# Optimization experiments

Measured on AMD Instinct MI355X. Metric: run time of the kernel, lower is better.

## Reference

```python
import jax, jax.numpy as jnp
import numpy as np

MI, DIS, DIN, HID, L, H, NG, H1, OUT = 2048, 1024, 3072, 256, 15, 8, 8, 512, 64
DENOM = 4.0 / 7.0  # (grid_max - grid_min) / (num_grids - 1)
EPS = 1e-5


def _ln(x, g, b):
    m = jnp.mean(x, axis=-1, keepdims=True)
    v = jnp.mean((x - m) ** 2, axis=-1, keepdims=True)
    return (x - m) * jax.lax.rsqrt(v + EPS) * g + b


def _fastkan(x, ln_g, ln_b, grid, Ws, Wb, bb):
    xn = _ln(x, ln_g, ln_b)
    basis = jnp.exp(-(((xn[..., None] - grid) / DENOM) ** 2))  # [N, DIN, NG]
    ret = basis.reshape(x.shape[0], -1) @ Ws.T                  # SplineLinear (no bias)
    return ret + jax.nn.silu(x) @ Wb.T + bb                      # base update


def _hgcn(x, G, W, attn, bias, rW1, rb1, rW2, rb2, ln_g, ln_b, jk_W, jk_b):
    # per-layer multi-head conv: mean_h a_h * G @ (x @ W_h) == G @ (x @ (sum_h a_h W_h / H))
    def step(xc, p):
        W_l, a_l, b_l, rW1_l, rb1_l, rW2_l, rb2_l, g_l, be_l = p
        W_eff = jnp.einsum('h,hio->io', a_l, W_l) / H
        out = G @ (xc @ W_eff) + b_l
        gate = jax.nn.sigmoid(jax.nn.relu(out @ rW1_l.T + rb1_l) @ rW2_l.T + rb2_l)
        out = _ln(out * gate, g_l, be_l)
        out = jnp.where(out >= 0, out, 0.25 * out)  # leaky_relu(0.25); dropout off (eval)
        return out, out
    _, outs = jax.lax.scan(step, x, (W, attn, bias, rW1, rb1, rW2, rb2, ln_g, ln_b))
    jk = jnp.moveaxis(outs, 0, 1).reshape(x.shape[0], L * HID)   # jumping-knowledge concat
    return jk @ jk_W.T + jk_b


def _mlp3(x, W1, b1, W2, b2, W3, b3):
    h = jax.nn.relu(x @ W1.T + b1)
    h = jax.nn.relu(h @ W2.T + b2)
    return jax.nn.relu(h @ W3.T + b3)


def _forward(concat_mi, concat_dis, G_mi, G_dis, AT, A, rbf_grid, mi_kan_ln_g, mi_kan_ln_b, mi_kan_Ws, mi_kan_Wb, mi_kan_bb, dis_kan_ln_g, dis_kan_ln_b, dis_kan_Ws, dis_kan_Wb, dis_kan_bb, mi_W, mi_attn, mi_bias, mi_rW1, mi_rb1, mi_rW2, mi_rb2, mi_ln_g, mi_ln_b, mi_jk_W, mi_jk_b, dis_W, dis_attn, dis_bias, dis_rW1, dis_rb1, dis_rW2, dis_rb2, dis_ln_g, dis_ln_b, dis_jk_W, dis_jk_b, lx_W1, lx_b1, lx_W2, lx_b2, lx_W3, lx_b3, ly_W1, ly_b1, ly_W2, ly_b2, ly_W3, ly_b3, ne_W, ne_b, he_W, he_b, mun_W, mun_b, mue_W, mue_b):
    # AT and A are accepted by the original forward but never used in its body.
    mi_e = _fastkan(concat_mi, mi_kan_ln_g, mi_kan_ln_b, rbf_grid, mi_kan_Ws, mi_kan_Wb, mi_kan_bb)
    dis_e = _fastkan(concat_dis, dis_kan_ln_g, dis_kan_ln_b, rbf_grid, dis_kan_Ws, dis_kan_Wb, dis_kan_bb)
    mi_f = _hgcn(mi_e, G_mi, mi_W, mi_attn, mi_bias, mi_rW1, mi_rb1, mi_rW2, mi_rb2, mi_ln_g, mi_ln_b, mi_jk_W, mi_jk_b)
    dis_f = _hgcn(dis_e, G_dis, dis_W, dis_attn, dis_bias, dis_rW1, dis_rb1, dis_rW2, dis_rb2, dis_ln_g, dis_ln_b, dis_jk_W, dis_jk_b)
    x = _mlp3(mi_f, lx_W1, lx_b1, lx_W2, lx_b2, lx_W3, lx_b3)
    y = _mlp3(dis_f, ly_W1, ly_b1, ly_W2, ly_b2, ly_W3, ly_b3)
    result_h = x @ y.T                                           # [MI, DIS]
    z_node = jax.nn.relu(concat_mi @ ne_W.T + ne_b)              # node_encoders1 (eval: no dropout)
    z_edge = jax.nn.relu(concat_dis @ he_W.T + he_b)             # hyperedge_encoders1
    z_node_mean = z_node @ mun_W.T + mun_b                       # _enc_mu_node (identity act)
    z_edge_mean = z_edge @ mue_W.T + mue_b                       # _enc_mu_hedge
    recon = z_node_mean @ z_edge_mean.T                          # decoder2 with identity act
    score = 0.7 * jax.nn.sigmoid(recon) + 0.3 * jax.nn.sigmoid(result_h)
    return score, recon


def setup_inputs() -> dict:
    ks = iter(jax.random.split(jax.random.key(0), 96))
    nrm = lambda shape, s: jax.random.normal(next(ks), shape, dtype=jnp.float32) * s
    uni = lambda shape: jax.random.uniform(next(ks), shape, dtype=jnp.float32)
    d = {}
    d['concat_mi'] = nrm((MI, DIN), 1.0)
    d['concat_dis'] = nrm((DIS, DIN), 1.0)
    d['G_mi'] = uni((MI, MI)) / MI    # row-normalized dense hypergraph adjacency
    d['G_dis'] = uni((DIS, DIS)) / DIS
    d['AT'] = uni((DIS, MI))
    d['A'] = uni((MI, DIS))
    d['rbf_grid'] = jnp.linspace(-2.0, 2.0, NG).astype(jnp.float32)
    for p in ('mi', 'dis'):
        d[p + '_kan_ln_g'] = jnp.ones((DIN,), jnp.float32)
        d[p + '_kan_ln_b'] = jnp.zeros((DIN,), jnp.float32)
        d[p + '_kan_Ws'] = nrm((HID, DIN * NG), 0.02)
        d[p + '_kan_Wb'] = nrm((HID, DIN), 0.02)
        d[p + '_kan_bb'] = nrm((HID,), 0.01)
        d[p + '_W'] = nrm((L, H, HID, HID), 0.06)
        d[p + '_attn'] = jnp.ones((L, H), jnp.float32)
        d[p + '_bias'] = nrm((L, HID), 0.01)
        d[p + '_rW1'] = nrm((L, HID // 4, HID), 0.05)
        d[p + '_rb1'] = nrm((L, HID // 4), 0.01)
        d[p + '_rW2'] = nrm((L, HID, HID // 4), 0.05)
        d[p + '_rb2'] = nrm((L, HID), 0.01)
        d[p + '_ln_g'] = jnp.ones((L, HID), jnp.float32)
        d[p + '_ln_b'] = jnp.zeros((L, HID), jnp.float32)
        d[p + '_jk_W'] = nrm((HID, L * HID), 0.02)
        d[p + '_jk_b'] = nrm((HID,), 0.01)
    for p in ('lx', 'ly'):
        d[p + '_W1'] = nrm((256, HID), 0.05); d[p + '_b1'] = nrm((256,), 0.01)
        d[p + '_W2'] = nrm((128, 256), 0.05); d[p + '_b2'] = nrm((128,), 0.01)
        d[p + '_W3'] = nrm((64, 128), 0.05); d[p + '_b3'] = nrm((64,), 0.01)
    d['ne_W'] = nrm((H1, DIN), 0.02); d['ne_b'] = nrm((H1,), 0.01)
    d['he_W'] = nrm((H1, DIN), 0.02); d['he_b'] = nrm((H1,), 0.01)
    d['mun_W'] = nrm((OUT, H1), 0.02); d['mun_b'] = nrm((OUT,), 0.01)
    d['mue_W'] = nrm((OUT, H1), 0.02); d['mue_b'] = nrm((OUT,), 0.01)
    return d


def reference(concat_mi, concat_dis, G_mi, G_dis, AT, A, rbf_grid, mi_kan_ln_g, mi_kan_ln_b, mi_kan_Ws, mi_kan_Wb, mi_kan_bb, dis_kan_ln_g, dis_kan_ln_b, dis_kan_Ws, dis_kan_Wb, dis_kan_bb, mi_W, mi_attn, mi_bias, mi_rW1, mi_rb1, mi_rW2, mi_rb2, mi_ln_g, mi_ln_b, mi_jk_W, mi_jk_b, dis_W, dis_attn, dis_bias, dis_rW1, dis_rb1, dis_rW2, dis_rb2, dis_ln_g, dis_ln_b, dis_jk_W, dis_jk_b, lx_W1, lx_b1, lx_W2, lx_b2, lx_W3, lx_b3, ly_W1, ly_b1, ly_W2, ly_b2, ly_W3, ly_b3, ne_W, ne_b, he_W, he_b, mun_W, mun_b, mue_W, mue_b):
    return _forward(concat_mi, concat_dis, G_mi, G_dis, AT, A, rbf_grid, mi_kan_ln_g, mi_kan_ln_b, mi_kan_Ws, mi_kan_Wb, mi_kan_bb, dis_kan_ln_g, dis_kan_ln_b, dis_kan_Ws, dis_kan_Wb, dis_kan_bb, mi_W, mi_attn, mi_bias, mi_rW1, mi_rb1, mi_rW2, mi_rb2, mi_ln_g, mi_ln_b, mi_jk_W, mi_jk_b, dis_W, dis_attn, dis_bias, dis_rW1, dis_rb1, dis_rW2, dis_rb2, dis_ln_g, dis_ln_b, dis_jk_W, dis_jk_b, lx_W1, lx_b1, lx_W2, lx_b2, lx_W3, lx_b3, ly_W1, ly_b1, ly_W2, ly_b2, ly_W3, ly_b3, ne_W, ne_b, he_W, he_b, mun_W, mun_b, mue_W, mue_b)
```

## Files before the change

kernel.cpp:

```cpp
#include <hip/hip_runtime.h>
#include <cstdint>
#include <cstddef>

typedef unsigned short u16;
typedef __attribute__((ext_vector_type(8))) short short8;
typedef __attribute__((ext_vector_type(4))) float f32x4;

#define MI_N  2048
#define DIS_N 1024
#define TOT_N 3072
#define DIN   3072
#define HID   256
#define LL    15
#define NG    8

__device__ __forceinline__ float b2f(u16 u) {
  unsigned int v = ((unsigned int)u) << 16;
  float f;
  __builtin_memcpy(&f, &v, 4);
  return f;
}
__device__ __forceinline__ u16 f2b(float f) {
  unsigned int u;
  __builtin_memcpy(&u, &f, 4);
  u = (u + 0x7fffu + ((u >> 16) & 1u)) >> 16;
  return (u16)u;
}
__device__ __forceinline__ float sigf(float x) { return 1.f / (1.f + __expf(-x)); }

#define NSEG 20
struct CvtJobs {
  const float* src[NSEG];
  u16* dst[NSEG];
  int nblk[NSEG];
  int nseg;
};

__global__ __launch_bounds__(256) void cvt_f2b(CvtJobs j) {
  int b = blockIdx.x, s = 0;
  while (s + 1 < j.nseg && b >= j.nblk[s]) { b -= j.nblk[s]; ++s; }
  const long base = ((long)b * 256 + threadIdx.x) * 8;
  const float4 v0 = *(const float4*)(j.src[s] + base);
  const float4 v1 = *(const float4*)(j.src[s] + base + 4);
  short8 o;
  o[0] = (short)f2b(v0.x); o[1] = (short)f2b(v0.y);
  o[2] = (short)f2b(v0.z); o[3] = (short)f2b(v0.w);
  o[4] = (short)f2b(v1.x); o[5] = (short)f2b(v1.y);
  o[6] = (short)f2b(v1.z); o[7] = (short)f2b(v1.w);
  *(short8*)(j.dst[s] + base) = o;
}

struct GP {
  const u16* A; int lda;
  const u16* B; int ldb;
  void* C; int ldc;
  const float* bias;
  int K;
  int mblk;
};

template <int ACT, int TRANS, int F32OUT, int NCT>
__global__ __launch_bounds__(256) void gemm_bt(GP p0, GP p1) {
  GP p = p0;
  int bx = blockIdx.x;
  if (bx >= p0.mblk) { bx -= p0.mblk; p = p1; }
  const int tid = threadIdx.x;
  const int w = tid >> 6;
  const int lane = tid & 63;
  const int m16 = lane & 15, quad = lane >> 4;
  const int kph = quad * 8;
  const long row0 = (long)bx * 32 + m16;
  const long colBase = (long)blockIdx.y * (16 * NCT);
  f32x4 acc[2][NCT] = {};
  const u16* A0 = p.A + row0 * (long)p.lda + kph;
  const u16* A1 = A0 + 16L * p.lda;
  const u16* Bb = p.B + (colBase + m16) * (long)p.ldb + kph;
  const long bstep = 16L * p.ldb;
  for (int kk = w * 32; kk < p.K; kk += 128) {
    short8 a0 = *(const short8*)(A0 + kk);
    short8 a1 = *(const short8*)(A1 + kk);
#pragma unroll
    for (int c = 0; c < NCT; ++c) {
      short8 b = *(const short8*)(Bb + c * bstep + kk);
      acc[0][c] = __builtin_amdgcn_mfma_f32_16x16x32_bf16(a0, b, acc[0][c], 0, 0, 0);
      acc[1][c] = __builtin_amdgcn_mfma_f32_16x16x32_bf16(a1, b, acc[1][c], 0, 0, 0);
    }
  }
  __shared__ float red[2][64][NCT * 8 + 1];
  float* av = (float*)acc;
  if (w >= 2) {
#pragma unroll
    for (int i = 0; i < NCT * 8; ++i) red[w - 2][lane][i] = av[i];
  }
  __syncthreads();
  if (w < 2) {
#pragma unroll
    for (int i = 0; i < NCT * 8; ++i) av[i] += red[w][lane][i];
  }
  __syncthreads();
  if (w == 1) {
#pragma unroll
    for (int i = 0; i < NCT * 8; ++i) red[0][lane][i] = av[i];
  }
  __syncthreads();
  if (w != 0) return;
#pragma unroll
  for (int i = 0; i < NCT * 8; ++i) av[i] += red[0][lane][i];
#pragma unroll
  for (int c = 0; c < NCT; ++c) {
    const long col = colBase + c * 16 + m16;
    const float bv = p.bias ? p.bias[col] : 0.f;
#pragma unroll
    for (int r = 0; r < 2; ++r) {
      const long orow = (long)bx * 32 + r * 16 + quad * 4;
#pragma unroll
      for (int j = 0; j < 4; ++j) {
        float v = acc[r][c][j] + bv;
        if (ACT == 1) v = fmaxf(v, 0.f);
        if (ACT == 2) v = sigf(v);
        if (F32OUT)
          ((float*)p.C)[(orow + j) * (long)p.ldc + col] = v;
        else if (TRANS)
          ((u16*)p.C)[col * (long)p.ldc + orow + j] = f2b(v);
        else
          ((u16*)p.C)[(orow + j) * (long)p.ldc + col] = f2b(v);
      }
    }
  }
}

struct FKP {
  const u16* xn; const u16* xb;
  const u16* Ws; const u16* Wb;
  float* partial;
  int rowoff;
  int mblk;
};

__global__ __launch_bounds__(256) void fastkan_gemm(FKP p0, FKP p1, const float* grid8) {
  FKP p = p0;
  int bx = blockIdx.x;
  if (bx >= p0.mblk) { bx -= p0.mblk; p = p1; }
  const int chunk = blockIdx.z;
  const int tid = threadIdx.x;
  const int w = tid >> 6;
  const int lane = tid & 63;
  const int m16 = lane & 15, quad = lane >> 4, kph = quad * 8;
  const long row0 = (long)bx * 32 + m16;
  const long colBase = (long)blockIdx.y * 128;
  f32x4 acc[2][8] = {};
  if (chunk < 4) {
    float gv[8];
#pragma unroll
    for (int j = 0; j < 8; ++j) gv[j] = grid8[j];
    const u16* xn0 = p.xn + row0 * (long)DIN;
    const u16* xn1 = xn0 + 16L * DIN;
    const int k0 = chunk * 6144, k1 = k0 + 6144;
    for (int kk = k0 + w * 32; kk < k1; kk += 128) {
      const int d = (kk >> 3) + quad;
      const float x0 = b2f(xn0[d]);
      const float x1 = b2f(xn1[d]);
      short8 a0, a1;
#pragma unroll
      for (int j = 0; j < 8; ++j) {
        float t0 = (x0 - gv[j]) * 1.75f;
        float t1 = (x1 - gv[j]) * 1.75f;
        a0[j] = (short)f2b(__expf(-t0 * t0));
        a1[j] = (short)f2b(__expf(-t1 * t1));
      }
#pragma unroll
      for (int c = 0; c < 8; ++c) {
        const u16* Bp = p.Ws + (colBase + c * 16 + m16) * (long)(DIN * NG) + kk + kph;
        short8 b = *(const short8*)Bp;
        acc[0][c] = __builtin_amdgcn_mfma_f32_16x16x32_bf16(a0, b, acc[0][c], 0, 0, 0);
        acc[1][c] = __builtin_amdgcn_mfma_f32_16x16x32_bf16(a1, b, acc[1][c], 0, 0, 0);
      }
    }
  } else {
    const u16* x0p = p.xb + row0 * (long)DIN + kph;
    const u16* x1p = x0p + 16L * DIN;
    for (int kk = w * 32; kk < DIN; kk += 128) {
      short8 r0 = *(const short8*)(x0p + kk);
      short8 r1 = *(const short8*)(x1p + kk);
      short8 a0, a1;
#pragma unroll
      for (int j = 0; j < 8; ++j) {
        float v0 = b2f((u16)r0[j]);
        float v1 = b2f((u16)r1[j]);
        a0[j] = (short)f2b(v0 * sigf(v0));
        a1[j] = (short)f2b(v1 * sigf(v1));
      }
#pragma unroll
      for (int c = 0; c < 8; ++c) {
        const u16* Bp = p.Wb + (colBase + c * 16 + m16) * (long)DIN + kk + kph;
        short8 b = *(const short8*)Bp;
        acc[0][c] = __builtin_amdgcn_mfma_f32_16x16x32_bf16(a0, b, acc[0][c], 0, 0, 0);
        acc[1][c] = __builtin_amdgcn_mfma_f32_16x16x32_bf16(a1, b, acc[1][c], 0, 0, 0);
      }
    }
  }
  __shared__ float red[2][64][65];
  float* av = (float*)acc;
  if (w >= 2) {
#pragma unroll
    for (int i = 0; i < 64; ++i) red[w - 2][lane][i] = av[i];
  }
  __syncthreads();
  if (w < 2) {
#pragma unroll
    for (int i = 0; i < 64; ++i) av[i] += red[w][lane][i];
  }
  __syncthreads();
  if (w == 1) {
#pragma unroll
    for (int i = 0; i < 64; ++i) red[0][lane][i] = av[i];
  }
  __syncthreads();
  if (w != 0) return;
#pragma unroll
  for (int i = 0; i < 64; ++i) av[i] += red[0][lane][i];
  float* outp = p.partial + ((long)chunk * TOT_N + p.rowoff) * HID;
#pragma unroll
  for (int c = 0; c < 8; ++c) {
    const long col = colBase + c * 16 + m16;
#pragma unroll
    for (int r = 0; r < 2; ++r) {
      const long orow = (long)bx * 32 + r * 16 + quad * 4;
#pragma unroll
      for (int j = 0; j < 4; ++j) outp[(orow + j) * HID + col] = acc[r][c][j];
    }
  }
}

__global__ __launch_bounds__(256) void fk_combine(const float* partial, const float* bb_mi,
                                                  const float* bb_dis, u16* e) {
  const long i = (long)blockIdx.x * 256 + threadIdx.x;
  const int c = (int)(i & 255);
  const long n = i >> 8;
  float s = 0.f;
#pragma unroll
  for (int pI = 0; pI < 5; ++pI) s += partial[(long)pI * TOT_N * HID + i];
  s += (n < MI_N ? bb_mi : bb_dis)[c];
  e[i] = f2b(s);
}

struct HLP {
  const u16* G; const u16* t1t; u16* t1t_next; const u16* weff_next;
  const float* bias; const u16* rw1; const float* rb1;
  const u16* rw2; const float* rb2; const float* lng; const float* lnb;
  u16* jk; int M; int mblk;
};

__global__ __launch_bounds__(256) void hgcn_layer(HLP p0, HLP p1) {
  HLP p = p0;
  int bx = blockIdx.x;
  if (bx >= p0.mblk) { bx -= p0.mblk; p = p1; }
  const int tid = threadIdx.x;
  const int w = tid >> 6, lane = tid & 63;
  const int m16 = lane & 15, quad = lane >> 4, kph = quad * 8;
  const int cb = w * 64;
  const long row0 = (long)bx * 32;
  __shared__ __align__(16) u16 hl[32][264];
  __shared__ __align__(16) u16 gl[32][264];
  __shared__ __align__(16) u16 g1l[32][72];

  {
    f32x4 acc[2][4] = {};
    const u16* A0 = p.G + (row0 + m16) * (long)p.M + kph;
    const u16* A1 = A0 + 16L * p.M;
    const u16* Bb = p.t1t + (long)(cb + m16) * p.M + kph;
    const long bstep = 16L * p.M;
    for (int kk = 0; kk < p.M; kk += 32) {
      short8 a0 = *(const short8*)(A0 + kk);
      short8 a1 = *(const short8*)(A1 + kk);
#pragma unroll
      for (int c = 0; c < 4; ++c) {
        short8 b = *(const short8*)(Bb + c * bstep + kk);
        acc[0][c] = __builtin_amdgcn_mfma_f32_16x16x32_bf16(a0, b, acc[0][c], 0, 0, 0);
        acc[1][c] = __builtin_amdgcn_mfma_f32_16x16x32_bf16(a1, b, acc[1][c], 0, 0, 0);
      }
    }
#pragma unroll
    for (int c = 0; c < 4; ++c) {
      const int col = cb + c * 16 + m16;
      const float bv = p.bias[col];
#pragma unroll
      for (int r = 0; r < 2; ++r) {
        const int orow = r * 16 + quad * 4;
#pragma unroll
        for (int j = 0; j < 4; ++j) hl[orow + j][col] = f2b(acc[r][c][j] + bv);
      }
    }
  }
  __syncthreads();
  {
    f32x4 acc[2] = {};
    const u16* Bb = p.rw1 + (long)(w * 16 + m16) * 256 + kph;
#pragma unroll
    for (int kk = 0; kk < 256; kk += 32) {
      short8 a0 = *(const short8*)&hl[m16][kk + kph];
      short8 a1 = *(const short8*)&hl[16 + m16][kk + kph];
      short8 b = *(const short8*)(Bb + kk);
      acc[0] = __builtin_amdgcn_mfma_f32_16x16x32_bf16(a0, b, acc[0], 0, 0, 0);
      acc[1] = __builtin_amdgcn_mfma_f32_16x16x32_bf16(a1, b, acc[1], 0, 0, 0);
    }
    const int col = w * 16 + m16;
    const float bv = p.rb1[col];
#pragma unroll
    for (int r = 0; r < 2; ++r) {
      const int orow = r * 16 + quad * 4;
#pragma unroll
      for (int j = 0; j < 4; ++j) g1l[orow + j][col] = f2b(fmaxf(acc[r][j] + bv, 0.f));
    }
  }
  __syncthreads();
  {
    f32x4 acc[2][4] = {};
    const u16* Bb = p.rw2 + (long)(cb + m16) * 64 + kph;
#pragma unroll
    for (int kk = 0; kk < 64; kk += 32) {
      short8 a0 = *(const short8*)&g1l[m16][kk + kph];
      short8 a1 = *(const short8*)&g1l[16 + m16][kk + kph];
#pragma unroll
      for (int c = 0; c < 4; ++c) {
        short8 b = *(const short8*)(Bb + c * (16L * 64) + kk);
        acc[0][c] = __builtin_amdgcn_mfma_f32_16x16x32_bf16(a0, b, acc[0][c], 0, 0, 0);
        acc[1][c] = __builtin_amdgcn_mfma_f32_16x16x32_bf16(a1, b, acc[1][c], 0, 0, 0);
      }
    }
#pragma unroll
    for (int c = 0; c < 4; ++c) {
      const int col = cb + c * 16 + m16;
      const float bv = p.rb2[col];
#pragma unroll
      for (int r = 0; r < 2; ++r) {
        const int orow = r * 16 + quad * 4;
#pragma unroll
        for (int j = 0; j < 4; ++j) gl[orow + j][col] = f2b(sigf(acc[r][c][j] + bv));
      }
    }
  }
  __syncthreads();
  {
    const int row = tid >> 3;
    const int sub = tid & 7;
    float pv[32];
    float s1 = 0.f, s2 = 0.f;
#pragma unroll
    for (int i = 0; i < 32; ++i) {
      const int col = sub * 32 + i;
      const float v = b2f(hl[row][col]) * b2f(gl[row][col]);
      pv[i] = v; s1 += v; s2 += v * v;
    }
#pragma unroll
    for (int o = 1; o < 8; o <<= 1) { s1 += __shfl_xor(s1, o); s2 += __shfl_xor(s2, o); }
    const float m = s1 * (1.f / HID);
    const float inv = rsqrtf(s2 * (1.f / HID) - m * m + 1e-5f);
    u16* jrow = p.jk + (row0 + row) * (long)(LL * HID);
#pragma unroll
    for (int i = 0; i < 32; ++i) {
      const int col = sub * 32 + i;
      float y = (pv[i] - m) * inv * p.lng[col] + p.lnb[col];
      y = (y >= 0.f) ? y : 0.25f * y;
      const u16 yb = f2b(y);
      jrow[col] = yb;
      gl[row][col] = yb;
    }
  }
  if (!p.weff_next) return;
  __syncthreads();
  {
    f32x4 acc[2][4] = {};
    const u16* Bb = p.weff_next + (long)(cb + m16) * 256 + kph;
#pragma unroll
    for (int kk = 0; kk < 256; kk += 32) {
      short8 a0 = *(const short8*)&gl[m16][kk + kph];
      short8 a1 = *(const short8*)&gl[16 + m16][kk + kph];
#pragma unroll
      for (int c = 0; c < 4; ++c) {
        short8 b = *(const short8*)(Bb + c * (16L * 256) + kk);
        acc[0][c] = __builtin_amdgcn_mfma_f32_16x16x32_bf16(a0, b, acc[0][c], 0, 0, 0);
        acc[1][c] = __builtin_amdgcn_mfma_f32_16x16x32_bf16(a1, b, acc[1][c], 0, 0, 0);
      }
    }
#pragma unroll
    for (int c = 0; c < 4; ++c) {
      const long col = cb + c * 16 + m16;
#pragma unroll
      for (int r = 0; r < 2; ++r) {
        const int orow = r * 16 + quad * 4;
#pragma unroll
        for (int j = 0; j < 4; ++j)
          p.t1t_next[col * (long)p.M + row0 + orow + j] = f2b(acc[r][c][j]);
      }
    }
  }
}

__global__ __launch_bounds__(256) void weff_kernel(const float* Wmi, const float* Ami,
                                                   const float* Wdis, const float* Adis,
                                                   u16* outT) {
  const int b = blockIdx.x;
  const int s = b / 3840;
  const int r = b % 3840;
  const int l = r >> 8;
  const int t = r & 255;
  const int i0 = (t >> 4) << 4;
  const int o0 = (t & 15) << 4;
  const float* W = (s ? Wdis : Wmi) + (long)l * 8 * 65536;
  const float* A = (s ? Adis : Ami) + l * 8;
  const int tx = threadIdx.x & 15;
  const int ty = threadIdx.x >> 4;
  float sum = 0.f;
#pragma unroll
  for (int h = 0; h < 8; ++h)
    sum += A[h] * W[(long)h * 65536 + (long)(i0 + ty) * 256 + o0 + tx];
  sum *= 0.125f;
  __shared__ float tile[16][17];
  tile[ty][tx] = sum;
  __syncthreads();
  outT[((long)s * LL + l) * 65536 + (long)(o0 + ty) * 256 + i0 + tx] = f2b(tile[tx][ty]);
}

__device__ __forceinline__ void breduce2(float& a, float& b) {
  for (int o = 32; o > 0; o >>= 1) {
    a += __shfl_down(a, o);
    b += __shfl_down(b, o);
  }
  __shared__ float sm[8];
  const int w = threadIdx.x >> 6;
  const int lane = threadIdx.x & 63;
  if (lane == 0) { sm[w] = a; sm[4 + w] = b; }
  __syncthreads();
  if (threadIdx.x == 0) {
    sm[0] = sm[0] + sm[1] + sm[2] + sm[3];
    sm[4] = sm[4] + sm[5] + sm[6] + sm[7];
  }
  __syncthreads();
  a = sm[0];
  b = sm[4];
}

__global__ __launch_bounds__(256) void ln_silu(const float* xmi, const float* xdis,
                                               const float* gmi, const float* bmi,
                                               const float* gdis, const float* bdis,
                                               u16* xn, u16* cbf) {
  const int n = blockIdx.x;
  const bool ds = (n >= MI_N);
  const float* x = ds ? xdis + (long)(n - MI_N) * DIN : xmi + (long)n * DIN;
  const float* g = ds ? gdis : gmi;
  const float* be = ds ? bdis : bmi;
  float xv[12];
  float s1 = 0.f, s2 = 0.f;
#pragma unroll
  for (int j = 0; j < 12; ++j) {
    xv[j] = x[j * 256 + threadIdx.x];
    s1 += xv[j];
    s2 += xv[j] * xv[j];
  }
  breduce2(s1, s2);
  const float m = s1 * (1.f / DIN);
  const float inv = rsqrtf(s2 * (1.f / DIN) - m * m + 1e-5f);
#pragma unroll
  for (int j = 0; j < 12; ++j) {
    const int e = j * 256 + threadIdx.x;
    xn[(long)n * DIN + e] = f2b((xv[j] - m) * inv * g[e] + be[e]);
    cbf[(long)n * DIN + e] = f2b(xv[j]);
  }
}

__global__ __launch_bounds__(256) void final_combine(const float* rh, float* out) {
  const long i = (long)blockIdx.x * 256 + threadIdx.x;
  const float rc = out[(long)MI_N * DIS_N + i];
  out[i] = 0.7f * sigf(rc) + 0.3f * sigf(rh[i]);
}

extern "C" void kernel_launch(void* const* d_in, const int* in_sizes, int n_in,
                              void* d_out, int out_size, void* d_ws, size_t ws_size,
                              hipStream_t stream) {
  const float* concat_mi   = (const float*)d_in[0];
  const float* concat_dis  = (const float*)d_in[1];
  const float* G_mi        = (const float*)d_in[2];
  const float* G_dis       = (const float*)d_in[3];
  const float* rbf_grid    = (const float*)d_in[6];
  const float* mi_kan_ln_g = (const float*)d_in[7];
  const float* mi_kan_ln_b = (const float*)d_in[8];
  const float* mi_kan_Ws   = (const float*)d_in[9];
  const float* mi_kan_Wb   = (const float*)d_in[10];
  const float* mi_kan_bb   = (const float*)d_in[11];
  const float* mi_W        = (const float*)d_in[12];
  const float* mi_attn     = (const float*)d_in[13];
  const float* mi_bias     = (const float*)d_in[14];
  const float* mi_rW1      = (const float*)d_in[15];
  const float* mi_rb1      = (const float*)d_in[16];
  const float* mi_rW2      = (const float*)d_in[17];
  const float* mi_rb2      = (const float*)d_in[18];
  const float* mi_ln_g     = (const float*)d_in[19];
  const float* mi_ln_b     = (const float*)d_in[20];
  const float* mi_jk_W     = (const float*)d_in[21];
  const float* mi_jk_b     = (const float*)d_in[22];
  const float* dis_kan_ln_g = (const float*)d_in[23];
  const float* dis_kan_ln_b = (const float*)d_in[24];
  const float* dis_kan_Ws  = (const float*)d_in[25];
  const float* dis_kan_Wb  = (const float*)d_in[26];
  const float* dis_kan_bb  = (const float*)d_in[27];
  const float* dis_W       = (const float*)d_in[28];
  const float* dis_attn    = (const float*)d_in[29];
  const float* dis_bias    = (const float*)d_in[30];
  const float* dis_rW1     = (const float*)d_in[31];
  const float* dis_rb1     = (const float*)d_in[32];
  const float* dis_rW2     = (const float*)d_in[33];
  const float* dis_rb2     = (const float*)d_in[34];
  const float* dis_ln_g    = (const float*)d_in[35];
  const float* dis_ln_b    = (const float*)d_in[36];
  const float* dis_jk_W    = (const float*)d_in[37];
  const float* dis_jk_b    = (const float*)d_in[38];
  const float* lx_W1 = (const float*)d_in[39]; const float* lx_b1 = (const float*)d_in[40];
  const float* lx_W2 = (const float*)d_in[41]; const float* lx_b2 = (const float*)d_in[42];
  const float* lx_W3 = (const float*)d_in[43]; const float* lx_b3 = (const float*)d_in[44];
  const float* ly_W1 = (const float*)d_in[45]; const float* ly_b1 = (const float*)d_in[46];
  const float* ly_W2 = (const float*)d_in[47]; const float* ly_b2 = (const float*)d_in[48];
  const float* ly_W3 = (const float*)d_in[49]; const float* ly_b3 = (const float*)d_in[50];
  const float* ne_W  = (const float*)d_in[51]; const float* ne_b  = (const float*)d_in[52];
  const float* he_W  = (const float*)d_in[53]; const float* he_b  = (const float*)d_in[54];
  const float* mun_W = (const float*)d_in[55]; const float* mun_b = (const float*)d_in[56];
  const float* mue_W = (const float*)d_in[57]; const float* mue_b = (const float*)d_in[58];

  char* wp = (char*)d_ws;
  size_t off = 0;
  auto alloc = [&](size_t bytes) -> void* {
    void* p = wp + off;
    off += (bytes + 255) & ~(size_t)255;
    return p;
  };
  u16* cbf    = (u16*)alloc((size_t)TOT_N * DIN * 2);
  u16* gmib   = (u16*)alloc((size_t)MI_N * MI_N * 2);
  u16* gdisb  = (u16*)alloc((size_t)DIS_N * DIS_N * 2);
  u16* wsb0   = (u16*)alloc((size_t)256 * 24576 * 2);
  u16* wsb1   = (u16*)alloc((size_t)256 * 24576 * 2);
  u16* wbb0   = (u16*)alloc((size_t)256 * 3072 * 2);
  u16* wbb1   = (u16*)alloc((size_t)256 * 3072 * 2);
  u16* jkwb0  = (u16*)alloc((size_t)256 * 3840 * 2);
  u16* jkwb1  = (u16*)alloc((size_t)256 * 3840 * 2);
  u16* rw1b0  = (u16*)alloc((size_t)LL * 64 * 256 * 2);
  u16* rw1b1  = (u16*)alloc((size_t)LL * 64 * 256 * 2);
  u16* rw2b0  = (u16*)alloc((size_t)LL * 256 * 64 * 2);
  u16* rw2b1  = (u16*)alloc((size_t)LL * 256 * 64 * 2);
  u16* lxw1b  = (u16*)alloc((size_t)256 * 256 * 2);
  u16* lxw2b  = (u16*)alloc((size_t)128 * 256 * 2);
  u16* lxw3b  = (u16*)alloc((size_t)64 * 128 * 2);
  u16* lyw1b  = (u16*)alloc((size_t)256 * 256 * 2);
  u16* lyw2b  = (u16*)alloc((size_t)128 * 256 * 2);
  u16* lyw3b  = (u16*)alloc((size_t)64 * 128 * 2);
  u16* neb    = (u16*)alloc((size_t)512 * 3072 * 2);
  u16* heb    = (u16*)alloc((size_t)512 * 3072 * 2);
  u16* munb   = (u16*)alloc((size_t)64 * 512 * 2);
  u16* mueb   = (u16*)alloc((size_t)64 * 512 * 2);
  u16* wefft  = (u16*)alloc((size_t)2 * LL * 65536 * 2);
  u16* e      = (u16*)alloc((size_t)TOT_N * HID * 2);
  u16* t1t    = (u16*)alloc((size_t)HID * TOT_N * 2);
  u16* t1t2   = (u16*)alloc((size_t)HID * TOT_N * 2);
  u16* jk     = (u16*)alloc((size_t)TOT_N * LL * HID * 2);
  u16* fb     = (u16*)alloc((size_t)TOT_N * HID * 2);
  char* regA  = (char*)alloc(35000000);
  u16* xn     = (u16*)regA;
  float* fkp  = (float*)(regA + 18874624);
  u16* h1b    = (u16*)regA;
  u16* h2b    = (u16*)(regA + 1572864);
  u16* xyb    = (u16*)(regA + 2359296);
  float* rh   = (float*)(regA + 2752512);
  u16* zb     = (u16*)(regA + 11141120);
  u16* zm     = (u16*)(regA + 14286848);
  float* outf = (float*)d_out;
  float* rec  = outf + (size_t)MI_N * DIS_N;
  (void)ws_size; (void)in_sizes; (void)n_in; (void)out_size;

  const dim3 B256(256);

  {
    CvtJobs cj{};
    int ns = 0, total = 0;
    auto push = [&](const float* s, u16* dst, int count) {
      cj.src[ns] = s; cj.dst[ns] = dst; cj.nblk[ns] = count / 2048;
      total += count / 2048; ++ns;
    };
    push(G_mi, gmib, MI_N * MI_N);
    push(G_dis, gdisb, DIS_N * DIS_N);
    push(mi_kan_Ws, wsb0, 256 * 24576);
    push(dis_kan_Ws, wsb1, 256 * 24576);
    push(mi_kan_Wb, wbb0, 256 * 3072);
    push(dis_kan_Wb, wbb1, 256 * 3072);
    push(mi_jk_W, jkwb0, 256 * 3840);
    push(dis_jk_W, jkwb1, 256 * 3840);
    push(mi_rW1, rw1b0, LL * 64 * 256);
    push(dis_rW1, rw1b1, LL * 64 * 256);
    push(mi_rW2, rw2b0, LL * 256 * 64);
    push(dis_rW2, rw2b1, LL * 256 * 64);
    push(lx_W1, lxw1b, 256 * 256);
    push(lx_W2, lxw2b, 128 * 256);
    push(lx_W3, lxw3b, 64 * 128);
    push(ly_W1, lyw1b, 256 * 256);
    push(ly_W2, lyw2b, 128 * 256);
    push(ly_W3, lyw3b, 64 * 128);
    push(ne_W, neb, 512 * 3072);
    push(he_W, heb, 512 * 3072);
    cj.nseg = ns;
    cvt_f2b<<<dim3(total), B256, 0, stream>>>(cj);
    CvtJobs cj2{};
    cj2.src[0] = mun_W; cj2.dst[0] = munb; cj2.nblk[0] = (64 * 512) / 2048;
    cj2.src[1] = mue_W; cj2.dst[1] = mueb; cj2.nblk[1] = (64 * 512) / 2048;
    cj2.nseg = 2;
    cvt_f2b<<<dim3(32), B256, 0, stream>>>(cj2);
  }
  ln_silu<<<dim3(TOT_N), B256, 0, stream>>>(concat_mi, concat_dis, mi_kan_ln_g, mi_kan_ln_b,
                                            dis_kan_ln_g, dis_kan_ln_b, xn, cbf);
  weff_kernel<<<dim3(2 * LL * 256), B256, 0, stream>>>(mi_W, mi_attn, dis_W, dis_attn, wefft);
  {
    FKP f0{xn, cbf, wsb0, wbb0, fkp, 0, 64};
    FKP f1{xn + (size_t)MI_N * DIN, cbf + (size_t)MI_N * DIN, wsb1, wbb1, fkp, MI_N, 32};
    fastkan_gemm<<<dim3(96, 2, 5), B256, 0, stream>>>(f0, f1, rbf_grid);
    fk_combine<<<dim3(TOT_N * HID / 256), B256, 0, stream>>>(fkp, mi_kan_bb, dis_kan_bb, e);
  }
  {
    GP a0{e, HID, wefft, 256, t1t, MI_N, nullptr, 256, 64};
    GP a1{e + (size_t)MI_N * HID, HID, wefft + (size_t)LL * 65536, 256,
          t1t + (size_t)HID * MI_N, DIS_N, nullptr, 256, 32};
    gemm_bt<0, 1, 0, 4><<<dim3(96, 4), B256, 0, stream>>>(a0, a1);
  }
  {
    u16* tc = t1t;
    u16* tn = t1t2;
    for (int l = 0; l < LL; ++l) {
      const bool last = (l == LL - 1);
      HLP h0{gmib, tc, tn, last ? nullptr : wefft + (size_t)(l + 1) * 65536,
             mi_bias + l * HID, rw1b0 + (size_t)l * 64 * HID, mi_rb1 + l * 64,
             rw2b0 + (size_t)l * HID * 64, mi_rb2 + l * HID,
             mi_ln_g + l * HID, mi_ln_b + l * HID, jk + (size_t)l * HID, MI_N, 64};
      HLP h1{gdisb, tc + (size_t)HID * MI_N, tn + (size_t)HID * MI_N,
             last ? nullptr : wefft + ((size_t)LL + l + 1) * 65536,
             dis_bias + l * HID, rw1b1 + (size_t)l * 64 * HID, dis_rb1 + l * 64,
             rw2b1 + (size_t)l * HID * 64, dis_rb2 + l * HID,
             dis_ln_g + l * HID, dis_ln_b + l * HID,
             jk + (size_t)MI_N * LL * HID + (size_t)l * HID, DIS_N, 32};
      hgcn_layer<<<dim3(96), B256, 0, stream>>>(h0, h1);
      u16* t = tc; tc = tn; tn = t;
    }
  }
  {
    GP j0{jk, LL * HID, jkwb0, LL * HID, fb, HID, mi_jk_b, LL * HID, 64};
    GP j1{jk + (size_t)MI_N * LL * HID, LL * HID, jkwb1, LL * HID, fb + (size_t)MI_N * HID,
          HID, dis_jk_b, LL * HID, 32};
    gemm_bt<0, 0, 0, 4><<<dim3(96, 4), B256, 0, stream>>>(j0, j1);
  }
  {
    GP m0{fb, HID, lxw1b, HID, h1b, 256, lx_b1, HID, 64};
    GP m1{fb + (size_t)MI_N * HID, HID, lyw1b, HID, h1b + (size_t)MI_N * 256, 256, ly_b1,
          HID, 32};
    gemm_bt<1, 0, 0, 4><<<dim3(96, 4), B256, 0, stream>>>(m0, m1);
    GP n0{h1b, 256, lxw2b, 256, h2b, 128, lx_b2, 256, 64};
    GP n1{h1b + (size_t)MI_N * 256, 256, lyw2b, 256, h2b + (size_t)MI_N * 128, 128, ly_b2,
          256, 32};
    gemm_bt<1, 0, 0, 4><<<dim3(96, 2), B256, 0, stream>>>(n0, n1);
    GP o0{h2b, 128, lxw3b, 128, xyb, 64, lx_b3, 128, 64};
    GP o1{h2b + (size_t)MI_N * 128, 128, lyw3b, 128, xyb + (size_t)MI_N * 64, 64, ly_b3,
          128, 32};
    gemm_bt<1, 0, 0, 4><<<dim3(96, 1), B256, 0, stream>>>(o0, o1);
  }
  {
    GP r0{xyb, 64, xyb + (size_t)MI_N * 64, 64, rh, DIS_N, nullptr, 64, 64};
    gemm_bt<0, 0, 1, 4><<<dim3(64, 16), B256, 0, stream>>>(r0, r0);
  }
  {
    GP e0{cbf, DIN, neb, DIN, zb, 512, ne_b, DIN, 64};
    GP e1{cbf + (size_t)MI_N * DIN, DIN, heb, DIN, zb + (size_t)MI_N * 512, 512, he_b, DIN,
          32};
    gemm_bt<1, 0, 0, 4><<<dim3(96, 8), B256, 0, stream>>>(e0, e1);
  }
  {
    GP u0{zb, 512, munb, 512, zm, 64, mun_b, 512, 64};
    GP u1{zb + (size_t)MI_N * 512, 512, mueb, 512, zm + (size_t)MI_N * 64, 64, mue_b, 512,
          32};
    gemm_bt<0, 0, 0, 4><<<dim3(96, 1), B256, 0, stream>>>(u0, u1);
  }
  {
    GP c0{zm, 64, zm + (size_t)MI_N * 64, 64, rec, DIS_N, nullptr, 64, 64};
    gemm_bt<0, 0, 1, 4><<<dim3(64, 16), B256, 0, stream>>>(c0, c0);
  }
  final_combine<<<dim3(MI_N * DIS_N / 256), B256, 0, stream>>>(rh, outf);
}
```

Before: 1.613 ms.

## Fuse all HGCN layers into one persistent cooperative kernel with grid barriers

Replaces the 15 per-layer hgcn_layer launches with a single cooperative kernel that loops over layers and uses an atomic grid barrier between them. Work is split into 192 blocks of 16 rows instead of 96 blocks of 32 rows, and the big G@t1 GEMM is split along K across the four waves, followed by an LDS reduction. The aim is to remove launch overhead and raise parallelism. In exchange it adds barrier cost, extra LDS reduction traffic and a spin-wait, and it relies on all blocks being co-resident if the plain-launch fallback is used.

```diff
diff --git a/kernel.cpp b/kernel.cpp
--- a/kernel.cpp
+++ b/kernel.cpp
@@ -13,6 +13,7 @@
 #define HID   256
 #define LL    15
 #define NG    8
+#define NBLK  192
 
 __device__ __forceinline__ float b2f(u16 u) {
   unsigned int v = ((unsigned int)u) << 16;
@@ -244,156 +245,202 @@
   e[i] = f2b(s);
 }
 
-struct HLP {
-  const u16* G; const u16* t1t; u16* t1t_next; const u16* weff_next;
-  const float* bias; const u16* rw1; const float* rb1;
-  const u16* rw2; const float* rb2; const float* lng; const float* lnb;
-  u16* jk; int M; int mblk;
+struct CoopP {
+  const u16* gmi; const u16* gdis; const u16* wefft;
+  u16* t1a; u16* t1b;
+  const float* bias_mi; const float* bias_dis;
+  const u16* rw1_mi; const u16* rw1_dis;
+  const u16* rw2_mi; const u16* rw2_dis;
+  const float* rb1_mi; const float* rb1_dis;
+  const float* rb2_mi; const float* rb2_dis;
+  const float* lng_mi; const float* lng_dis;
+  const float* lnb_mi; const float* lnb_dis;
+  u16* jk;
+  unsigned* bar;
 };
 
-__global__ __launch_bounds__(256) void hgcn_layer(HLP p0, HLP p1) {
-  HLP p = p0;
-  int bx = blockIdx.x;
-  if (bx >= p0.mblk) { bx -= p0.mblk; p = p1; }
+__device__ __forceinline__ void grid_sync(unsigned* bar) {
+  __syncthreads();
+  if (threadIdx.x == 0) {
+    __threadfence();
+    const unsigned g = atomicAdd(&bar[1], 0u);
+    const unsigned a = atomicAdd(&bar[0], 1u) + 1u;
+    if (a == (unsigned)NBLK) {
+      atomicExch(&bar[0], 0u);
+      atomicAdd(&bar[1], 1u);
+    } else {
+      while (atomicAdd(&bar[1], 0u) == g) __builtin_amdgcn_s_sleep(8);
+    }
+    __threadfence();
+  }
+  __syncthreads();
+}
+
+__global__ __launch_bounds__(256) void hgcn_all(CoopP p) {
+  const int b = blockIdx.x;
   const int tid = threadIdx.x;
   const int w = tid >> 6, lane = tid & 63;
   const int m16 = lane & 15, quad = lane >> 4, kph = quad * 8;
   const int cb = w * 64;
-  const long row0 = (long)bx * 32;
-  __shared__ __align__(16) u16 hl[32][264];
-  __shared__ __align__(16) u16 gl[32][264];
-  __shared__ __align__(16) u16 g1l[32][72];
-
-  {
-    f32x4 acc[2][4] = {};
-    const u16* A0 = p.G + (row0 + m16) * (long)p.M + kph;
-    const u16* A1 = A0 + 16L * p.M;
-    const u16* Bb = p.t1t + (long)(cb + m16) * p.M + kph;
-    const long bstep = 16L * p.M;
-    for (int kk = 0; kk < p.M; kk += 32) {
-      short8 a0 = *(const short8*)(A0 + kk);
-      short8 a1 = *(const short8*)(A1 + kk);
+  const bool mi = (b < 128);
+  const int M = mi ? MI_N : DIS_N;
+  const int row0 = mi ? b * 16 : (b - 128) * 16;
+  const long grow = mi ? row0 : (long)MI_N + row0;
+  const u16* G = mi ? p.gmi : p.gdis;
+
+  __shared__ float red[2][64][65];
+  __shared__ __align__(16) u16 hl[16][264];
+  __shared__ __align__(16) u16 g1l[16][72];
+  __shared__ __align__(16) u16 gl[16][264];
+
+  u16* tc = p.t1a;
+  u16* tn = p.t1b;
+
+  for (int l = 0; l < LL; ++l) {
+    const float* bias = (mi ? p.bias_mi : p.bias_dis) + l * HID;
+    const u16* rw1 = (mi ? p.rw1_mi : p.rw1_dis) + (size_t)l * 64 * HID;
+    const float* rb1 = (mi ? p.rb1_mi : p.rb1_dis) + l * 64;
+    const u16* rw2 = (mi ? p.rw2_mi : p.rw2_dis) + (size_t)l * HID * 64;
+    const float* rb2 = (mi ? p.rb2_mi : p.rb2_dis) + l * HID;
+    const float* lng = (mi ? p.lng_mi : p.lng_dis) + l * HID;
+    const float* lnb = (mi ? p.lnb_mi : p.lnb_dis) + l * HID;
+    const u16* tb = mi ? tc : tc + (size_t)HID * MI_N;
+
+    {
+      f32x4 acc[16] = {};
+      const u16* A = G + (long)(row0 + m16) * M + kph;
+      const u16* Bc = tb + (long)m16 * M + kph;
+      const int kbase = w * (M >> 2);
+      const int it1 = M >> 7;
+#pragma unroll 4
+      for (int kk = 0; kk < it1; ++kk) {
+        const int ka = kbase + kk * 32;
+        short8 a = *(const short8*)(A + ka);
+#pragma unroll
+        for (int c = 0; c < 16; ++c) {
+          short8 bb = *(const short8*)(Bc + (long)c * 16 * M + ka);
+          acc[c] = __builtin_amdgcn_mfma_f32_16x16x32_bf16(a, bb, acc[c], 0, 0, 0);
+        }
+      }
+      float* av = (float*)acc;
+      if (w >= 2) {
+#pragma unroll
+        for (int i = 0; i < 64; ++i) red[w - 2][lane][i] = av[i];
+      }
+      __syncthreads();
+      if (w < 2) {
+#pragma unroll
+        for (int i = 0; i < 64; ++i) av[i] += red[w][lane][i];
+      }
+      __syncthreads();
+      if (w == 1) {
+#pragma unroll
+        for (int i = 0; i < 64; ++i) red[0][lane][i] = av[i];
+      }
+      __syncthreads();
+      if (w == 0) {
+#pragma unroll
+        for (int i = 0; i < 64; ++i) av[i] += red[0][lane][i];
+#pragma unroll
+        for (int c = 0; c < 16; ++c) {
+          const int col = c * 16 + m16;
+          const float bv = bias[col];
+#pragma unroll
+          for (int j = 0; j < 4; ++j) hl[quad * 4 + j][col] = f2b(acc[c][j] + bv);
+        }
+      }
+      __syncthreads();
+    }
+    {
+      f32x4 acc = {};
+      const u16* Bb = rw1 + (long)(w * 16 + m16) * 256 + kph;
+#pragma unroll
+      for (int kk = 0; kk < 256; kk += 32) {
+        short8 a = *(const short8*)&hl[m16][kk + kph];
+        short8 bb = *(const short8*)(Bb + kk);
+        acc = __builtin_amdgcn_mfma_f32_16x16x32_bf16(a, bb, acc, 0, 0, 0);
+      }
+      const int col = w * 16 + m16;
+      const float bv = rb1[col];
+#pragma unroll
+      for (int j = 0; j < 4; ++j) g1l[quad * 4 + j][col] = f2b(fmaxf(acc[j] + bv, 0.f));
+    }
+    __syncthreads();
+    {
+      f32x4 acc[4] = {};
+      const u16* Bb = rw2 + (long)(cb + m16) * 64 + kph;
+#pragma unroll
+      for (int kk = 0; kk < 64; kk += 32) {
+        short8 a = *(const short8*)&g1l[m16][kk + kph];
+#pragma unroll
+        for (int c = 0; c < 4; ++c) {
+          short8 bb = *(const short8*)(Bb + c * (16L * 64) + kk);
+          acc[c] = __builtin_amdgcn_mfma_f32_16x16x32_bf16(a, bb, acc[c], 0, 0, 0);
+        }
+      }
 #pragma unroll
       for (int c = 0; c < 4; ++c) {
-        short8 b = *(const short8*)(Bb + c * bstep + kk);
-        acc[0][c] = __builtin_amdgcn_mfma_f32_16x16x32_bf16(a0, b, acc[0][c], 0, 0, 0);
-        acc[1][c] = __builtin_amdgcn_mfma_f32_16x16x32_bf16(a1, b, acc[1][c], 0, 0, 0);
-      }
-    }
-#pragma unroll
-    for (int c = 0; c < 4; ++c) {
-      const int col = cb + c * 16 + m16;
-      const float bv = p.bias[col];
-#pragma unroll
-      for (int r = 0; r < 2; ++r) {
-        const int orow = r * 16 + quad * 4;
-#pragma unroll
-        for (int j = 0; j < 4; ++j) hl[orow + j][col] = f2b(acc[r][c][j] + bv);
-      }
-    }
-  }
-  __syncthreads();
-  {
-    f32x4 acc[2] = {};
-    const u16* Bb = p.rw1 + (long)(w * 16 + m16) * 256 + kph;
-#pragma unroll
-    for (int kk = 0; kk < 256; kk += 32) {
-      short8 a0 = *(const short8*)&hl[m16][kk + kph];
-      short8 a1 = *(const short8*)&hl[16 + m16][kk + kph];
-      short8 b = *(const short8*)(Bb + kk);
-      acc[0] = __builtin_amdgcn_mfma_f32_16x16x32_bf16(a0, b, acc[0], 0, 0, 0);
-      acc[1] = __builtin_amdgcn_mfma_f32_16x16x32_bf16(a1, b, acc[1], 0, 0, 0);
-    }
-    const int col = w * 16 + m16;
-    const float bv = p.rb1[col];
-#pragma unroll
-    for (int r = 0; r < 2; ++r) {
-      const int orow = r * 16 + quad * 4;
-#pragma unroll
-      for (int j = 0; j < 4; ++j) g1l[orow + j][col] = f2b(fmaxf(acc[r][j] + bv, 0.f));
-    }
-  }
-  __syncthreads();
-  {
-    f32x4 acc[2][4] = {};
-    const u16* Bb = p.rw2 + (long)(cb + m16) * 64 + kph;
-#pragma unroll
-    for (int kk = 0; kk < 64; kk += 32) {
-      short8 a0 = *(const short8*)&g1l[m16][kk + kph];
-      short8 a1 = *(const short8*)&g1l[16 + m16][kk + kph];
+        const int col = cb + c * 16 + m16;
+        const float bv = rb2[col];
+#pragma unroll
+        for (int j = 0; j < 4; ++j) gl[quad * 4 + j][col] = f2b(sigf(acc[c][j] + bv));
+      }
+    }
+    __syncthreads();
+    {
+      const int row = tid >> 4, sub = tid & 15;
+      float pv[16];
+      float s1 = 0.f, s2 = 0.f;
+#pragma unroll
+      for (int i = 0; i < 16; ++i) {
+        const int col = sub * 16 + i;
+        const float v = b2f(hl[row][col]) * b2f(gl[row][col]);
+        pv[i] = v; s1 += v; s2 += v * v;
+      }
+#pragma unroll
+      for (int o = 1; o < 16; o <<= 1) {
+        s1 += __shfl_xor(s1, o);
+        s2 += __shfl_xor(s2, o);
+      }
+      const float m = s1 * (1.f / HID);
+      const float inv = rsqrtf(s2 * (1.f / HID) - m * m + 1e-5f);
+      u16* jrow = p.jk + (size_t)(grow + row) * (LL * HID) + (size_t)l * HID;
+#pragma unroll
+      for (int i = 0; i < 16; ++i) {
+        const int col = sub * 16 + i;
+        float y = (pv[i] - m) * inv * lng[col] + lnb[col];
+        y = (y >= 0.f) ? y : 0.25f * y;
+        const u16 yb = f2b(y);
+        jrow[col] = yb;
+        gl[row][col] = yb;
+      }
+    }
+    if (l == LL - 1) break;
+    __syncthreads();
+    {
+      const u16* weff_nx = p.wefft + ((mi ? 0 : LL) + l + 1) * (size_t)65536;
+      u16* to = mi ? tn : tn + (size_t)HID * MI_N;
+      f32x4 acc[4] = {};
+      const u16* Bb = weff_nx + (long)(cb + m16) * 256 + kph;
+#pragma unroll
+      for (int kk = 0; kk < 256; kk += 32) {
+        short8 a = *(const short8*)&gl[m16][kk + kph];
+#pragma unroll
+        for (int c = 0; c < 4; ++c) {
+          short8 bb = *(const short8*)(Bb + c * (16L * 256) + kk);
+          acc[c] = __builtin_amdgcn_mfma_f32_16x16x32_bf16(a, bb, acc[c], 0, 0, 0);
+        }
+      }
 #pragma unroll
       for (int c = 0; c < 4; ++c) {
-        short8 b = *(const short8*)(Bb + c * (16L * 64) + kk);
-        acc[0][c] = __builtin_amdgcn_mfma_f32_16x16x32_bf16(a0, b, acc[0][c], 0, 0, 0);
-        acc[1][c] = __builtin_amdgcn_mfma_f32_16x16x32_bf16(a1, b, acc[1][c], 0, 0, 0);
-      }
-    }
-#pragma unroll
-    for (int c = 0; c < 4; ++c) {
-      const int col = cb + c * 16 + m16;
-      const float bv = p.rb2[col];
-#pragma unroll
-      for (int r = 0; r < 2; ++r) {
-        const int orow = r * 16 + quad * 4;
-#pragma unroll
-        for (int j = 0; j < 4; ++j) gl[orow + j][col] = f2b(sigf(acc[r][c][j] + bv));
-      }
-    }
-  }
-  __syncthreads();
-  {
-    const int row = tid >> 3;
-    const int sub = tid & 7;
-    float pv[32];
-    float s1 = 0.f, s2 = 0.f;
-#pragma unroll
-    for (int i = 0; i < 32; ++i) {
-      const int col = sub * 32 + i;
-      const float v = b2f(hl[row][col]) * b2f(gl[row][col]);
-      pv[i] = v; s1 += v; s2 += v * v;
-    }
-#pragma unroll
-    for (int o = 1; o < 8; o <<= 1) { s1 += __shfl_xor(s1, o); s2 += __shfl_xor(s2, o); }
-    const float m = s1 * (1.f / HID);
-    const float inv = rsqrtf(s2 * (1.f / HID) - m * m + 1e-5f);
-    u16* jrow = p.jk + (row0 + row) * (long)(LL * HID);
-#pragma unroll
-    for (int i = 0; i < 32; ++i) {
-      const int col = sub * 32 + i;
-      float y = (pv[i] - m) * inv * p.lng[col] + p.lnb[col];
-      y = (y >= 0.f) ? y : 0.25f * y;
-      const u16 yb = f2b(y);
-      jrow[col] = yb;
-      gl[row][col] = yb;
-    }
-  }
-  if (!p.weff_next) return;
-  __syncthreads();
-  {
-    f32x4 acc[2][4] = {};
-    const u16* Bb = p.weff_next + (long)(cb + m16) * 256 + kph;
-#pragma unroll
-    for (int kk = 0; kk < 256; kk += 32) {
-      short8 a0 = *(const short8*)&gl[m16][kk + kph];
-      short8 a1 = *(const short8*)&gl[16 + m16][kk + kph];
-#pragma unroll
-      for (int c = 0; c < 4; ++c) {
-        short8 b = *(const short8*)(Bb + c * (16L * 256) + kk);
-        acc[0][c] = __builtin_amdgcn_mfma_f32_16x16x32_bf16(a0, b, acc[0][c], 0, 0, 0);
-        acc[1][c] = __builtin_amdgcn_mfma_f32_16x16x32_bf16(a1, b, acc[1][c], 0, 0, 0);
-      }
-    }
-#pragma unroll
-    for (int c = 0; c < 4; ++c) {
-      const long col = cb + c * 16 + m16;
-#pragma unroll
-      for (int r = 0; r < 2; ++r) {
-        const int orow = r * 16 + quad * 4;
+        const long col = cb + c * 16 + m16;
 #pragma unroll
         for (int j = 0; j < 4; ++j)
-          p.t1t_next[col * (long)p.M + row0 + orow + j] = f2b(acc[r][c][j]);
-      }
-    }
+          to[col * (long)M + row0 + quad * 4 + j] = f2b(acc[c][j]);
+      }
+    }
+    grid_sync(p.bar);
+    u16* t = tc; tc = tn; tn = t;
   }
 }
 
@@ -562,6 +609,7 @@
   u16* t1t2   = (u16*)alloc((size_t)HID * TOT_N * 2);
   u16* jk     = (u16*)alloc((size_t)TOT_N * LL * HID * 2);
   u16* fb     = (u16*)alloc((size_t)TOT_N * HID * 2);
+  unsigned* barp = (unsigned*)alloc(256);
   char* regA  = (char*)alloc(35000000);
   u16* xn     = (u16*)regA;
   float* fkp  = (float*)(regA + 18874624);
@@ -628,22 +676,16 @@
     gemm_bt<0, 1, 0, 4><<<dim3(96, 4), B256, 0, stream>>>(a0, a1);
   }
   {
-    u16* tc = t1t;
-    u16* tn = t1t2;
-    for (int l = 0; l < LL; ++l) {
-      const bool last = (l == LL - 1);
-      HLP h0{gmib, tc, tn, last ? nullptr : wefft + (size_t)(l + 1) * 65536,
-             mi_bias + l * HID, rw1b0 + (size_t)l * 64 * HID, mi_rb1 + l * 64,
-             rw2b0 + (size_t)l * HID * 64, mi_rb2 + l * HID,
-             mi_ln_g + l * HID, mi_ln_b + l * HID, jk + (size_t)l * HID, MI_N, 64};
-      HLP h1{gdisb, tc + (size_t)HID * MI_N, tn + (size_t)HID * MI_N,
-             last ? nullptr : wefft + ((size_t)LL + l + 1) * 65536,
-             dis_bias + l * HID, rw1b1 + (size_t)l * 64 * HID, dis_rb1 + l * 64,
-             rw2b1 + (size_t)l * HID * 64, dis_rb2 + l * HID,
-             dis_ln_g + l * HID, dis_ln_b + l * HID,
-             jk + (size_t)MI_N * LL * HID + (size_t)l * HID, DIS_N, 32};
-      hgcn_layer<<<dim3(96), B256, 0, stream>>>(h0, h1);
-      u16* t = tc; tc = tn; tn = t;
+    hipMemsetAsync(barp, 0, 256, stream);
+    CoopP cp{gmib, gdisb, wefft, t1t, t1t2, mi_bias, dis_bias,
+             rw1b0, rw1b1, rw2b0, rw2b1, mi_rb1, dis_rb1, mi_rb2, dis_rb2,
+             mi_ln_g, dis_ln_g, mi_ln_b, dis_ln_b, jk, barp};
+    void* kp[] = {(void*)&cp};
+    hipError_t cerr = hipLaunchCooperativeKernel(
+        reinterpret_cast<const void*>(&hgcn_all), dim3(NBLK), dim3(256), kp, 0u, stream);
+    if (cerr != hipSuccess) {
+      (void)hipGetLastError();
+      hgcn_all<<<dim3(NBLK), B256, 0, stream>>>(cp);
     }
   }
   {
```

Result: slower. 1.691 ms (+4.8%).
